# Kernel optimization log

Hardware: AMD Instinct MI355X
Metric: run time of the kernel (lower is better)

The kernel has to match this reference:

```python
import jax, jax.numpy as jnp
import numpy as np

N, E, H, HEADS, L, B = 16000, 256000, 192, 4, 4, 8
C = H // HEADS
VN, VE, T = 32, 8, 1000


def _sin_emb(t, dim):
    half = dim // 2
    freqs = jnp.exp(-np.log(10000.0) * jnp.arange(half, dtype=jnp.float32) / half)
    ang = t.astype(jnp.float32)[:, None] * freqs[None, :]
    return jnp.concatenate([jnp.sin(ang), jnp.cos(ang)], axis=-1)


def _ln(x, g, b, eps=1e-5):
    mu = jnp.mean(x, -1, keepdims=True)
    var = jnp.mean(jnp.square(x - mu), -1, keepdims=True)
    return (x - mu) * jax.lax.rsqrt(var + eps) * g + b


def setup_inputs():
    key = jax.random.key(0)
    ks = iter(jax.random.split(key, 64))
    p = lambda shape, s=0.02: jax.random.normal(next(ks), shape, jnp.float32) * s
    inp = {}
    inp['node_emb'] = p((VN, H))
    inp['edge_emb'] = p((VE, H))
    inp['time_w1'] = p((H, H)); inp['time_b1'] = jnp.zeros((H,), jnp.float32)
    inp['time_w2'] = p((H, H)); inp['time_b2'] = jnp.zeros((H,), jnp.float32)
    inp['mask_emb'] = p((2, H))
    inp['wq'] = p((L, H, H)); inp['bq'] = jnp.zeros((L, H), jnp.float32)
    inp['wk'] = p((L, H, H)); inp['bk'] = jnp.zeros((L, H), jnp.float32)
    inp['wv'] = p((L, H, H)); inp['bv'] = jnp.zeros((L, H), jnp.float32)
    inp['we'] = p((L, H, H))
    inp['wskip'] = p((L, H, H)); inp['bskip'] = jnp.zeros((L, H), jnp.float32)
    inp['wbeta'] = p((L, 3 * H))
    inp['ln_g'] = jnp.ones((L, H), jnp.float32); inp['ln_b'] = jnp.zeros((L, H), jnp.float32)
    inp['node_out_w'] = p((H, VN)); inp['node_out_b'] = jnp.zeros((VN,), jnp.float32)
    inp['edge_w1'] = p((4 * H, H)); inp['edge_b1'] = jnp.zeros((H,), jnp.float32)
    inp['edge_w2'] = p((H, VE)); inp['edge_b2'] = jnp.zeros((VE,), jnp.float32)
    inp['node_type'] = jax.random.randint(next(ks), (N,), 0, VN)
    inp['edge_type'] = jax.random.randint(next(ks), (E,), 0, VE)
    inp['edge_index'] = jax.random.randint(next(ks), (2, E), 0, N)
    inp['edit_mask'] = jax.random.randint(next(ks), (N,), 0, 2, dtype=jnp.int32)
    inp['node_batch'] = jnp.sort(jax.random.randint(next(ks), (N,), 0, B))
    inp['t_graph'] = jax.random.randint(next(ks), (B,), 1, T)
    return inp


def reference(node_emb, edge_emb, time_w1, time_b1, time_w2, time_b2, mask_emb,
              wq, bq, wk, bk, wv, bv, we, wskip, bskip, wbeta, ln_g, ln_b,
              node_out_w, node_out_b, edge_w1, edge_b1, edge_w2, edge_b2,
              node_type, edge_type, edge_index, edit_mask, node_batch, t_graph):
    src, dst = edge_index[0], edge_index[1]
    # time embedding: sinusoidal -> Linear -> SiLU -> Linear  => [B, H]
    t_vec = jax.nn.silu(_sin_emb(t_graph, H) @ time_w1 + time_b1) @ time_w2 + time_b2
    t_node = t_vec[node_batch]              # [N, H]
    t_edge = t_vec[node_batch[src]]         # [E, H]
    x = node_emb[node_type] + t_node + mask_emb[edit_mask]
    edge_attr = edge_emb[edge_type] + t_edge
    scale = 1.0 / np.sqrt(C)
    for l in range(L):
        q = (x @ wq[l] + bq[l]).reshape(N, HEADS, C)
        k = (x @ wk[l] + bk[l]).reshape(N, HEADS, C)
        v = (x @ wv[l] + bv[l]).reshape(N, HEADS, C)
        e = (edge_attr @ we[l]).reshape(E, HEADS, C)
        kj = k[src] + e                                   # [E, heads, C]
        score = jnp.sum(q[dst] * kj, axis=-1) * scale      # [E, heads]
        m = jax.ops.segment_max(score, dst, num_segments=N)
        ex = jnp.exp(score - m[dst])
        denom = jax.ops.segment_sum(ex, dst, num_segments=N)
        alpha = ex / denom[dst]
        msg = (v[src] + e) * alpha[..., None]              # [E, heads, C]
        out = jax.ops.segment_sum(msg, dst, num_segments=N).reshape(N, H)
        xr = x @ wskip[l] + bskip[l]
        beta = jax.nn.sigmoid(jnp.concatenate([out, xr, out - xr], -1) @ wbeta[l])[:, None]
        h = beta * xr + (1.0 - beta) * out
        x = _ln(x + h, ln_g[l], ln_b[l])
    node_logits = x @ node_out_w + node_out_b
    edge_feat = jnp.concatenate([x[src], x[dst], edge_attr, t_edge], -1)  # [E, 4H]
    edge_logits = jax.nn.silu(edge_feat @ edge_w1 + edge_b1) @ edge_w2 + edge_b2
    return node_logits, edge_logits
```

## Files before the change

### kernel.cpp

```cpp
#include <hip/hip_runtime.h>
#include <hip/hip_bf16.h>
#include <math.h>

#define NN 16000
#define NPAD 16128
#define NE 256000
#define H 192
#define RP 256
#define KVR 512
#define NL 4
#define NBATCH 8
#define VEt 8
#define HH (H*H)
#define EML 16

typedef __hip_bfloat16 bf16;
typedef unsigned short u16;
typedef unsigned char u8;
typedef unsigned int u32;
typedef __attribute__((ext_vector_type(8))) short bfrag_t;
typedef __attribute__((ext_vector_type(4))) float facc_t;
typedef __attribute__((ext_vector_type(4))) float f4;
typedef __attribute__((ext_vector_type(2))) unsigned int u32x2;

__device__ __forceinline__ bf16 f2b(float v){ return __float2bfloat16(v); }

__device__ __forceinline__ unsigned enc8sw(float x){
    unsigned u = __float_as_uint(x);
    unsigned s = (u >> 24) & 0x80u;
    float ax = fabsf(x);
    if(ax >= 448.f) return s | 0x7Eu;
    if(ax < 0.015625f){
        int q = (int)rintf(ax * 512.f);
        return s | (unsigned)q;
    }
    unsigned au = u & 0x7FFFFFFFu;
    unsigned lsb = (au >> 20) & 1u;
    au += 0x7FFFFu + lsb;
    unsigned E = (au >> 23) - 127u;
    unsigned M = (au >> 20) & 7u;
    if((int)E > 8) return s | 0x7Eu;
    return s | ((E + 7u) << 3) | M;
}
__device__ __forceinline__ unsigned enc8(float x){
#if __has_builtin(__builtin_amdgcn_cvt_pk_fp8_f32)
    return (u32)__builtin_amdgcn_cvt_pk_fp8_f32(x, x, 0, false) & 0xFFu;
#else
    return enc8sw(x);
#endif
}
template<int SEL>
__device__ __forceinline__ float dec8s(u32 w){
#if __has_builtin(__builtin_amdgcn_cvt_f32_fp8)
    return __builtin_amdgcn_cvt_f32_fp8((int)w, SEL);
#else
    unsigned v = (w >> (SEL*8)) & 0xFFu;
    unsigned e = (v >> 3) & 15u, m = v & 7u;
    float mag = e ? __builtin_ldexpf((float)(8u + m), (int)e - 10)
                  : __builtin_ldexpf((float)m, -9);
    return (v & 0x80u) ? -mag : mag;
#endif
}
__device__ __forceinline__ float frcp(float x){
#if __has_builtin(__builtin_amdgcn_rcpf)
    return __builtin_amdgcn_rcpf(x);
#else
    return 1.f/x;
#endif
}

__global__ void k_sentinel(float* __restrict__ out, float v){ out[0] = v; }

__global__ void k_transpose(const float* __restrict__ wq, const float* __restrict__ wk,
                            const float* __restrict__ wv, const float* __restrict__ wsk,
                            const float* __restrict__ w1, u16* __restrict__ wt){
    int mat = blockIdx.x;
    const float* src;
    if(mat < 4)       src = wq  + (size_t)mat*HH;
    else if(mat < 8)  src = wk  + (size_t)(mat-4)*HH;
    else if(mat < 12) src = wv  + (size_t)(mat-8)*HH;
    else if(mat < 16) src = wsk + (size_t)(mat-12)*HH;
    else              src = w1  + (size_t)(mat-16)*HH;
    u16* dst = wt + (size_t)mat*HH;
    const int slice = HH/8;
    int base = blockIdx.y*slice;
    for(int i = base + threadIdx.x; i < base + slice; i += blockDim.x){
        int k = i / H, n = i % H;
        bf16 b = f2b(src[i]);
        dst[n*H + k] = *(u16*)&b;
    }
}

__global__ void k_tvec(const int* __restrict__ tg, const float* __restrict__ w1,
                       const float* __restrict__ b1, const float* __restrict__ w2,
                       const float* __restrict__ b2, float* __restrict__ tvec){
    int b = blockIdx.x, j = threadIdx.x;
    __shared__ float emb[H], h1[H];
    float t = (float)tg[b];
    if(j < 96){
        float fr = __expf(-logf(10000.0f) * (float)j / 96.0f);
        float ang = t * fr;
        emb[j]      = sinf(ang);
        emb[j + 96] = cosf(ang);
    }
    __syncthreads();
    float acc = b1[j];
    for(int k = 0; k < H; k++) acc += emb[k] * w1[k*H + j];
    h1[j] = acc / (1.f + __expf(-acc));
    __syncthreads();
    float acc2 = b2[j];
    for(int k = 0; k < H; k++) acc2 += h1[k] * w2[k*H + j];
    tvec[b*H + j] = acc2;
}

__global__ void k_init_x(const float* __restrict__ nemb, const float* __restrict__ memb,
                         const float* __restrict__ tvec, const int* __restrict__ ntype,
                         const int* __restrict__ emask, const int* __restrict__ nbatch,
                         float* __restrict__ x, u16* __restrict__ xb){
    int idx = blockIdx.x*blockDim.x + threadIdx.x;
    if(idx >= NN*H) return;
    int n = idx / H, c = idx % H;
    float v = nemb[(size_t)ntype[n]*H + c] + tvec[nbatch[n]*H + c]
            + memb[(size_t)emask[n]*H + c];
    x[idx] = v;
    bf16 b = f2b(v); xb[idx] = *(u16*)&b;
}

__global__ void k_zero_i(int* __restrict__ p, int n){
    int i = blockIdx.x*blockDim.x + threadIdx.x;
    if(i < n) p[i] = 0;
}
__global__ void k_count(const int* __restrict__ edst, int* __restrict__ cnt){
    int e = blockIdx.x*blockDim.x + threadIdx.x;
    if(e < NE) atomicAdd(&cnt[edst[e]], 1);
}
__global__ __launch_bounds__(1024) void k_scan(const int* __restrict__ cnt,
                                               int* __restrict__ ofs, int* __restrict__ cur){
    __shared__ int wsum[16];
    __shared__ int carry_s;
    int tid = threadIdx.x, lane = tid & 63, w = tid >> 6;
    if(tid == 0) carry_s = 0;
    __syncthreads();
    for(int base = 0; base < NN; base += 1024){
        int idx = base + tid;
        int v = (idx < NN) ? cnt[idx] : 0;
        int sc = v;
        #pragma unroll
        for(int o = 1; o < 64; o <<= 1){
            int t = __shfl_up(sc, o);
            if(lane >= o) sc += t;
        }
        if(lane == 63) wsum[w] = sc;
        __syncthreads();
        if(w == 0){
            int ws = (lane < 16) ? wsum[lane] : 0;
            #pragma unroll
            for(int o = 1; o < 16; o <<= 1){
                int t = __shfl_up(ws, o);
                if(lane >= o) ws += t;
            }
            if(lane < 16) wsum[lane] = ws;
        }
        __syncthreads();
        int wbase = (w > 0) ? wsum[w-1] : 0;
        int c = carry_s;
        int excl = c + wbase + sc - v;
        if(idx < NN){ ofs[idx] = excl; cur[idx] = excl; }
        __syncthreads();
        if(tid == 0) carry_s = c + wsum[15];
        __syncthreads();
    }
    if(threadIdx.x == 0) ofs[NN] = carry_s;
}
__global__ void k_scatter(const int* __restrict__ esrc, const int* __restrict__ edst,
                          const int* __restrict__ etype, const int* __restrict__ nbatch,
                          int* __restrict__ cur, int2* __restrict__ spair){
    int e = blockIdx.x*blockDim.x + threadIdx.x;
    if(e >= NE) return;
    int s = esrc[e], d = edst[e];
    int pos = atomicAdd(&cur[d], 1);
    int2 se; se.x = s; se.y = nbatch[s]*VEt + etype[e];
    spair[pos] = se;
}

__global__ void k_etab(const float* __restrict__ eemb, const float* __restrict__ tvec,
                       const float* __restrict__ we, u16* __restrict__ etab){
    int blk = blockIdx.x;
    int l = blk >> 6, idx = blk & 63, b = idx >> 3, et = idx & 7;
    int c = threadIdx.x;
    __shared__ float a[H];
    a[c] = eemb[et*H + c] + tvec[b*H + c];
    __syncthreads();
    float acc = 0.f;
    const float* w = we + (size_t)l*HH;
    for(int k = 0; k < H; k++) acc += a[k] * w[k*H + c];
    bf16 bv = f2b(acc);
    etab[(size_t)blk*256 + (c/3)*4 + (c%3)] = *(u16*)&bv;
}

__global__ void k_ctab(const float* __restrict__ eemb, const float* __restrict__ tvec,
                       const float* __restrict__ w1, const float* __restrict__ b1,
                       float* __restrict__ ctab){
    int idx = blockIdx.x, b = idx >> 3, et = idx & 7;
    int c = threadIdx.x;
    __shared__ float a[H];
    a[c] = eemb[et*H + c] + tvec[b*H + c];
    __syncthreads();
    float acc = b1[c];
    for(int k = 0; k < H; k++){
        acc += a[k]          * w1[(size_t)(2*H + k)*H + c];
        acc += tvec[b*H + k] * w1[(size_t)(3*H + k)*H + c];
    }
    ctab[(size_t)idx*RP + (c/3)*4 + (c%3)] = acc;
}

struct GemmP {
    const u16* wt[4];
    const float* bias[4];
    void* out[4];
    int obf[4];
};
__global__ __launch_bounds__(256) void k_gemm(const u16* __restrict__ A, GemmP P){
    int oi = blockIdx.y / 3, nt = blockIdx.y % 3;
    const u16* Wt = P.wt[oi];
    const float* bias = P.bias[oi];
    int wave = threadIdx.x >> 6, lane = threadIdx.x & 63;
    int quad = lane >> 4, l16 = lane & 15;
    int m0 = blockIdx.x*256 + wave*64;
    int n0 = nt*64;
    facc_t acc[4][4];
    #pragma unroll
    for(int i = 0; i < 4; i++)
        #pragma unroll
        for(int j = 0; j < 4; j++){ acc[i][j][0]=0.f; acc[i][j][1]=0.f; acc[i][j][2]=0.f; acc[i][j][3]=0.f; }
    #pragma unroll
    for(int kc = 0; kc < 6; kc++){
        int kb = kc*32 + quad*8;
        bfrag_t af[4], bg[4];
        #pragma unroll
        for(int i = 0; i < 4; i++) af[i] = *(const bfrag_t*)(A  + (size_t)(m0 + i*16 + l16)*H + kb);
        #pragma unroll
        for(int j = 0; j < 4; j++) bg[j] = *(const bfrag_t*)(Wt + (size_t)(n0 + j*16 + l16)*H + kb);
        #pragma unroll
        for(int i = 0; i < 4; i++)
            #pragma unroll
            for(int j = 0; j < 4; j++)
                acc[i][j] = __builtin_amdgcn_mfma_f32_16x16x32_bf16(af[i], bg[j], acc[i][j], 0, 0, 0);
    }
    float bv[4];
    #pragma unroll
    for(int j = 0; j < 4; j++) bv[j] = bias ? bias[n0 + j*16 + l16] : 0.f;
    int mode = P.obf[oi];
    if(mode != 0){
        u8* out = (u8*)P.out[oi];
        int rstride = (mode == 2) ? RP : KVR;
        int mult    = (mode == 2) ? 4  : 8;
        int koff    = (mode == 4) ? 4  : 0;
        int byteoff[4];
        #pragma unroll
        for(int j = 0; j < 4; j++){
            int c = n0 + j*16 + l16;
            byteoff[j] = (c/3)*mult + (c%3) + koff;
        }
        #pragma unroll
        for(int i = 0; i < 4; i++){
            int rb = m0 + i*16 + quad*4;
            #pragma unroll
            for(int r = 0; r < 4; r++){
                int row = rb + r;
                if(row < NN){
                    #pragma unroll
                    for(int j = 0; j < 4; j++)
                        out[(size_t)row*rstride + byteoff[j]] = (u8)enc8(acc[i][j][r] + bv[j]);
                }
            }
        }
    } else {
        float* out = (float*)P.out[oi];
        #pragma unroll
        for(int i = 0; i < 4; i++){
            int rb = m0 + i*16 + quad*4;
            #pragma unroll
            for(int r = 0; r < 4; r++){
                int row = rb + r;
                if(row < NN){
                    #pragma unroll
                    for(int j = 0; j < 4; j++)
                        out[(size_t)row*H + n0 + j*16 + l16] = acc[i][j][r] + bv[j];
                }
            }
        }
    }
}

__global__ __launch_bounds__(256) void k_attn(
    const float* __restrict__ Q, const u8* __restrict__ KVb,
    const float* __restrict__ XR,
    const u16* __restrict__ etab, const int* __restrict__ ofs,
    const int2* __restrict__ spair,
    const float* __restrict__ wb, const float* __restrict__ lng, const float* __restrict__ lnb,
    float* __restrict__ x, u16* __restrict__ xb)
{
    int n = blockIdx.x*4 + (threadIdx.x >> 6);
    int lane = threadIdx.x & 63;
    int ch = lane*3;
    size_t base = (size_t)n*H + ch;
    const float scale = 0.14433756729740646f;
    float q0 = Q[base], q1 = Q[base+1], q2 = Q[base+2];
    int p0 = ofs[n], p1 = ofs[n+1];
    float lac[4]  = {0.f,0.f,0.f,0.f};
    float ac0[4]  = {0.f,0.f,0.f,0.f};
    float ac1[4]  = {0.f,0.f,0.f,0.f};
    float ac2[4]  = {0.f,0.f,0.f,0.f};
    const u8* etb = (const u8*)etab;
    int p = p0;
    for(; p + 3 < p1; p += 4){
        int s[4], ei[4];
        #pragma unroll
        for(int t = 0; t < 4; t++){ int2 se = spair[p+t]; s[t] = se.x; ei[t] = se.y; }
        u32x2 kv[4], ew[4];
        #pragma unroll
        for(int t = 0; t < 4; t++){
            kv[t] = *(const u32x2*)(KVb + (size_t)s[t]*KVR + lane*8);
            ew[t] = *(const u32x2*)(etb + (size_t)ei[t]*KVR + lane*8);
        }
        float e0[4], e1[4], e2[4], tt[4];
        #pragma unroll
        for(int t = 0; t < 4; t++){
            e0[t] = __uint_as_float(ew[t].x << 16);
            e1[t] = __uint_as_float(ew[t].x & 0xffff0000u);
            e2[t] = __uint_as_float(ew[t].y << 16);
            tt[t] = q0*(dec8s<0>(kv[t].x)+e0[t]) + q1*(dec8s<1>(kv[t].x)+e1[t])
                  + q2*(dec8s<2>(kv[t].x)+e2[t]);
        }
        #pragma unroll
        for(int o = 1; o <= 8; o <<= 1){
            #pragma unroll
            for(int t = 0; t < 4; t++) tt[t] += __shfl_xor(tt[t], o);
        }
        #pragma unroll
        for(int t = 0; t < 4; t++){
            float sc = fminf(fmaxf(tt[t]*scale, -60.f), 60.f);
            float pw = __expf(sc);
            lac[t] += pw;
            ac0[t] += pw*(dec8s<0>(kv[t].y)+e0[t]);
            ac1[t] += pw*(dec8s<1>(kv[t].y)+e1[t]);
            ac2[t] += pw*(dec8s<2>(kv[t].y)+e2[t]);
        }
    }
    for(; p < p1; p++){
        int2 se = spair[p];
        u32x2 kvA = *(const u32x2*)(KVb + (size_t)se.x*KVR + lane*8);
        u32x2 ewA = *(const u32x2*)(etb + (size_t)se.y*KVR + lane*8);
        float e0A = __uint_as_float(ewA.x << 16);
        float e1A = __uint_as_float(ewA.x & 0xffff0000u);
        float e2A = __uint_as_float(ewA.y << 16);
        float tA = q0*(dec8s<0>(kvA.x)+e0A) + q1*(dec8s<1>(kvA.x)+e1A) + q2*(dec8s<2>(kvA.x)+e2A);
        tA += __shfl_xor(tA,1); tA += __shfl_xor(tA,2); tA += __shfl_xor(tA,4); tA += __shfl_xor(tA,8);
        float sc = fminf(fmaxf(tA*scale, -60.f), 60.f);
        float pw = __expf(sc);
        lac[0] += pw;
        ac0[0] += pw*(dec8s<0>(kvA.y)+e0A);
        ac1[0] += pw*(dec8s<1>(kvA.y)+e1A);
        ac2[0] += pw*(dec8s<2>(kvA.y)+e2A);
    }
    float l  = (lac[0]+lac[1]) + (lac[2]+lac[3]);
    float a0 = (ac0[0]+ac0[1]) + (ac0[2]+ac0[3]);
    float a1 = (ac1[0]+ac1[1]) + (ac1[2]+ac1[3]);
    float a2 = (ac2[0]+ac2[1]) + (ac2[2]+ac2[3]);
    float inv = (p1 > p0) ? 1.f/l : 0.f;
    float o0 = a0*inv, o1 = a1*inv, o2 = a2*inv;
    float xr0 = XR[base], xr1 = XR[base+1], xr2 = XR[base+2];
    float sd = o0*wb[ch]  + o1*wb[ch+1]  + o2*wb[ch+2]
             + xr0*wb[H+ch] + xr1*wb[H+ch+1] + xr2*wb[H+ch+2]
             + (o0-xr0)*wb[2*H+ch] + (o1-xr1)*wb[2*H+ch+1] + (o2-xr2)*wb[2*H+ch+2];
    sd += __shfl_xor(sd,1); sd += __shfl_xor(sd,2); sd += __shfl_xor(sd,4);
    sd += __shfl_xor(sd,8); sd += __shfl_xor(sd,16); sd += __shfl_xor(sd,32);
    float beta = 1.f/(1.f + __expf(-sd));
    float h0 = beta*xr0 + (1.f-beta)*o0;
    float h1 = beta*xr1 + (1.f-beta)*o1;
    float h2 = beta*xr2 + (1.f-beta)*o2;
    float y0 = x[base] + h0, y1 = x[base+1] + h1, y2 = x[base+2] + h2;
    float s3 = y0 + y1 + y2;
    s3 += __shfl_xor(s3,1); s3 += __shfl_xor(s3,2); s3 += __shfl_xor(s3,4);
    s3 += __shfl_xor(s3,8); s3 += __shfl_xor(s3,16); s3 += __shfl_xor(s3,32);
    float mean = s3 * (1.f/H);
    float d0 = y0-mean, d1 = y1-mean, d2 = y2-mean;
    float v3 = d0*d0 + d1*d1 + d2*d2;
    v3 += __shfl_xor(v3,1); v3 += __shfl_xor(v3,2); v3 += __shfl_xor(v3,4);
    v3 += __shfl_xor(v3,8); v3 += __shfl_xor(v3,16); v3 += __shfl_xor(v3,32);
    float rs = rsqrtf(v3*(1.f/H) + 1e-5f);
    float z0 = d0*rs*lng[ch]   + lnb[ch];
    float z1 = d1*rs*lng[ch+1] + lnb[ch+1];
    float z2 = d2*rs*lng[ch+2] + lnb[ch+2];
    x[base] = z0; x[base+1] = z1; x[base+2] = z2;
    bf16 t0 = f2b(z0), t1 = f2b(z1), t2 = f2b(z2);
    xb[base] = *(u16*)&t0; xb[base+1] = *(u16*)&t1; xb[base+2] = *(u16*)&t2;
}

__global__ void k_nodeout(const float* __restrict__ x, const float* __restrict__ w,
                          const float* __restrict__ b, float* __restrict__ out){
    int j = threadIdx.x & 31;
    int n = blockIdx.x*8 + (threadIdx.x >> 5);
    float acc = b[j];
    const float* xr = x + (size_t)n*H;
    for(int k = 0; k < H; k++) acc += xr[k] * w[k*32 + j];
    out[(size_t)n*32 + j] = acc;
}

__global__ __launch_bounds__(256) void k_edgemlp(
    const int* __restrict__ esrc, const int* __restrict__ edst, const int* __restrict__ etype,
    const int* __restrict__ nb,
    const u8* __restrict__ xs1, const u8* __restrict__ xd1, const float* __restrict__ ctab,
    const float* __restrict__ w2, const float* __restrict__ b2p, float* __restrict__ out)
{
    int wid = blockIdx.x*4 + (threadIdx.x >> 6);
    int lane = threadIdx.x & 63;
    int ch = lane*3;
    float w2r[3][8];
    #pragma unroll
    for(int t = 0; t < 3; t++)
        #pragma unroll
        for(int j = 0; j < 8; j++) w2r[t][j] = w2[(ch+t)*8 + j];
    int jout = (lane&1)*4 + (lane&2) + ((lane&4)>>2);
    float bo = (lane < 8) ? b2p[jout] : 0.f;
    int b0 = lane & 1, b1 = lane & 2, b2m = lane & 4;
    int e0 = wid*EML;
    for(int eb = e0; eb < e0 + EML; eb += 2){
        int sX = esrc[eb],   dX = edst[eb];
        int sY = esrc[eb+1], dY = edst[eb+1];
        int ctX = nb[sX]*VEt + etype[eb];
        int ctY = nb[sY]*VEt + etype[eb+1];
        u32 awX = *(const u32*)(xs1 + (size_t)sX*RP + lane*4);
        u32 awY = *(const u32*)(xs1 + (size_t)sY*RP + lane*4);
        u32 bwX = *(const u32*)(xd1 + (size_t)dX*RP + lane*4);
        u32 bwY = *(const u32*)(xd1 + (size_t)dY*RP + lane*4);
        f4  cfX = *(const f4*)(ctab + (size_t)ctX*RP + lane*4);
        f4  cfY = *(const f4*)(ctab + (size_t)ctY*RP + lane*4);
        float hX0, hX1, hX2, hY0, hY1, hY2;
        { float v = dec8s<0>(awX)+dec8s<0>(bwX)+cfX.x; hX0 = v*frcp(1.f+__expf(-v)); }
        { float v = dec8s<1>(awX)+dec8s<1>(bwX)+cfX.y; hX1 = v*frcp(1.f+__expf(-v)); }
        { float v = dec8s<2>(awX)+dec8s<2>(bwX)+cfX.z; hX2 = v*frcp(1.f+__expf(-v)); }
        { float v = dec8s<0>(awY)+dec8s<0>(bwY)+cfY.x; hY0 = v*frcp(1.f+__expf(-v)); }
        { float v = dec8s<1>(awY)+dec8s<1>(bwY)+cfY.y; hY1 = v*frcp(1.f+__expf(-v)); }
        { float v = dec8s<2>(awY)+dec8s<2>(bwY)+cfY.z; hY2 = v*frcp(1.f+__expf(-v)); }
        float pjX[8], pjY[8];
        #pragma unroll
        for(int j = 0; j < 8; j++){
            pjX[j] = hX0*w2r[0][j] + hX1*w2r[1][j] + hX2*w2r[2][j];
            pjY[j] = hY0*w2r[0][j] + hY1*w2r[1][j] + hY2*w2r[2][j];
        }
        float v4X[4], v4Y[4];
        #pragma unroll
        for(int t = 0; t < 4; t++){
            float sX4 = b0 ? pjX[t] : pjX[t+4];
            float kX4 = b0 ? pjX[t+4] : pjX[t];
            v4X[t] = kX4 + __shfl_xor(sX4, 1);
            float sY4 = b0 ? pjY[t] : pjY[t+4];
            float kY4 = b0 ? pjY[t+4] : pjY[t];
            v4Y[t] = kY4 + __shfl_xor(sY4, 1);
        }
        float v2X[2], v2Y[2];
        #pragma unroll
        for(int t = 0; t < 2; t++){
            float sX2 = b1 ? v4X[t] : v4X[t+2];
            float kX2 = b1 ? v4X[t+2] : v4X[t];
            v2X[t] = kX2 + __shfl_xor(sX2, 2);
            float sY2 = b1 ? v4Y[t] : v4Y[t+2];
            float kY2 = b1 ? v4Y[t+2] : v4Y[t];
            v2Y[t] = kY2 + __shfl_xor(sY2, 2);
        }
        float v1X, v1Y;
        {
            float sX1 = b2m ? v2X[0] : v2X[1];
            float kX1 = b2m ? v2X[1] : v2X[0];
            v1X = kX1 + __shfl_xor(sX1, 4);
            float sY1 = b2m ? v2Y[0] : v2Y[1];
            float kY1 = b2m ? v2Y[1] : v2Y[0];
            v1Y = kY1 + __shfl_xor(sY1, 4);
        }
        v1X += __shfl_xor(v1X, 8);  v1Y += __shfl_xor(v1Y, 8);
        v1X += __shfl_xor(v1X, 16); v1Y += __shfl_xor(v1Y, 16);
        v1X += __shfl_xor(v1X, 32); v1Y += __shfl_xor(v1Y, 32);
        if(lane < 8){
            out[(size_t)eb*8 + jout]     = v1X + bo;
            out[(size_t)(eb+1)*8 + jout] = v1Y + bo;
        }
    }
}

extern "C" void kernel_launch(void* const* d_in, const int* in_sizes, int n_in,
                              void* d_out, int out_size, void* d_ws, size_t ws_size,
                              hipStream_t stream)
{
    {
        int bad = -1;
        if(n_in != 31) bad = 100;
        else {
            const int chk_idx[9] = {0, 7, 16, 21, 23, 26, 27, 29, 30};
            const int chk_sz [9] = {32*H, NL*HH, NL*3*H, 4*HH, H*8, NE, 2*NE, NN, NBATCH};
            for(int i = 0; i < 9; i++) if(in_sizes[chk_idx[i]] != chk_sz[i]){ bad = chk_idx[i]; break; }
        }
        if(bad >= 0){ k_sentinel<<<1,1,0,stream>>>((float*)d_out, 20000.f + 256.f*bad); return; }
        if(out_size != NN*32 + NE*8){ k_sentinel<<<1,1,0,stream>>>((float*)d_out, 30000.f); return; }
    }

    const float* node_emb = (const float*)d_in[0];
    const float* edge_emb = (const float*)d_in[1];
    const float* time_w1  = (const float*)d_in[2];
    const float* time_b1  = (const float*)d_in[3];
    const float* time_w2  = (const float*)d_in[4];
    const float* time_b2  = (const float*)d_in[5];
    const float* mask_emb = (const float*)d_in[6];
    const float* wq       = (const float*)d_in[7];
    const float* bq       = (const float*)d_in[8];
    const float* wk       = (const float*)d_in[9];
    const float* bk       = (const float*)d_in[10];
    const float* wv       = (const float*)d_in[11];
    const float* bv       = (const float*)d_in[12];
    const float* we       = (const float*)d_in[13];
    const float* wskip    = (const float*)d_in[14];
    const float* bskip    = (const float*)d_in[15];
    const float* wbeta    = (const float*)d_in[16];
    const float* ln_g     = (const float*)d_in[17];
    const float* ln_b     = (const float*)d_in[18];
    const float* now      = (const float*)d_in[19];
    const float* nob      = (const float*)d_in[20];
    const float* ew1      = (const float*)d_in[21];
    const float* eb1      = (const float*)d_in[22];
    const float* ew2      = (const float*)d_in[23];
    const float* eb2      = (const float*)d_in[24];
    const int* node_type  = (const int*)d_in[25];
    const int* edge_type  = (const int*)d_in[26];
    const int* edge_index = (const int*)d_in[27];
    const int* edit_mask  = (const int*)d_in[28];
    const int* node_batch = (const int*)d_in[29];
    const int* t_graph    = (const int*)d_in[30];
    const int* esrc = edge_index;
    const int* edst = edge_index + NE;

    char* wsb = (char*)d_ws;
    size_t off = 0;
    auto take = [&](size_t bytes) -> char* {
        char* r = wsb + off;
        off += (bytes + 255) & ~(size_t)255;
        return r;
    };
    float* tvec = (float*)take((size_t)NBATCH*H*4);
    float* x    = (float*)take((size_t)NN*H*4);
    u16*   xb   = (u16*)  take((size_t)NPAD*H*2);
    float* Q    = (float*)take((size_t)NN*H*4);
    u8*    KVb  = (u8*)   take((size_t)NN*KVR);
    float* XR   = (float*)take((size_t)NN*H*4);
    u8*    xs1  = (u8*)   take((size_t)NN*RP);
    u8*    xd1  = (u8*)   take((size_t)NN*RP);
    u16*   etab = (u16*)  take((size_t)NL*64*KVR);
    float* ctab = (float*)take((size_t)64*RP*4);
    u16*   wt   = (u16*)  take((size_t)18*HH*2);
    int* cnt    = (int*)  take((size_t)(NN+1)*4);
    int* offa   = (int*)  take((size_t)(NN+1)*4);
    int* cur    = (int*)  take((size_t)(NN+1)*4);
    int2* spair = (int2*) take((size_t)NE*8);

    if(ws_size < off){
        k_sentinel<<<1,1,0,stream>>>((float*)d_out, 10000.f + (float)(ws_size >> 20));
        return;
    }

    k_transpose<<<dim3(18, 8), 256, 0, stream>>>(wq, wk, wv, wskip, ew1, wt);
    k_tvec<<<NBATCH, H, 0, stream>>>(t_graph, time_w1, time_b1, time_w2, time_b2, tvec);
    k_init_x<<<(NN*H + 255)/256, 256, 0, stream>>>(node_emb, mask_emb, tvec, node_type,
                                                   edit_mask, node_batch, x, xb);
    k_zero_i<<<(NN + 255)/256, 256, 0, stream>>>(cnt, NN);
    k_count<<<NE/256, 256, 0, stream>>>(edst, cnt);
    k_scan<<<1, 1024, 0, stream>>>(cnt, offa, cur);
    k_scatter<<<NE/256, 256, 0, stream>>>(esrc, edst, edge_type, node_batch, cur, spair);
    k_etab<<<NL*64, H, 0, stream>>>(edge_emb, tvec, we, etab);
    k_ctab<<<64, H, 0, stream>>>(edge_emb, tvec, ew1, eb1, ctab);

    for(int l = 0; l < NL; l++){
        GemmP P;
        P.wt[0] = wt + (size_t)(0  + l)*HH;  P.bias[0] = bq   + (size_t)l*H;  P.out[0] = Q;   P.obf[0] = 0;
        P.wt[1] = wt + (size_t)(4  + l)*HH;  P.bias[1] = bk   + (size_t)l*H;  P.out[1] = KVb; P.obf[1] = 3;
        P.wt[2] = wt + (size_t)(8  + l)*HH;  P.bias[2] = bv   + (size_t)l*H;  P.out[2] = KVb; P.obf[2] = 4;
        P.wt[3] = wt + (size_t)(12 + l)*HH;  P.bias[3] = bskip+ (size_t)l*H;  P.out[3] = XR;  P.obf[3] = 0;
        k_gemm<<<dim3(63, 12), 256, 0, stream>>>(xb, P);
        k_attn<<<NN/4, 256, 0, stream>>>(Q, KVb, XR, etab + (size_t)l*64*256, offa, spair,
                                         wbeta + (size_t)l*3*H, ln_g + (size_t)l*H,
                                         ln_b + (size_t)l*H, x, xb);
    }
    {
        GemmP P;
        P.wt[0] = wt + (size_t)16*HH; P.bias[0] = nullptr; P.out[0] = xs1; P.obf[0] = 2;
        P.wt[1] = wt + (size_t)17*HH; P.bias[1] = nullptr; P.out[1] = xd1; P.obf[1] = 2;
        P.wt[2] = P.wt[0]; P.bias[2] = nullptr; P.out[2] = xs1; P.obf[2] = 2;
        P.wt[3] = P.wt[0]; P.bias[3] = nullptr; P.out[3] = xs1; P.obf[3] = 2;
        k_gemm<<<dim3(63, 6), 256, 0, stream>>>(xb, P);
    }
    k_nodeout<<<NN/8, 256, 0, stream>>>(x, now, nob, (float*)d_out);
    k_edgemlp<<<NE/(4*EML), 256, 0, stream>>>(esrc, edst, edge_type, node_batch, xs1, xd1, ctab,
                                              ew2, eb2, (float*)d_out + (size_t)NN*32);
}
```

Measured before the change: 537.6 us.

## Use bf16 MFMA for node output projection and edge MLP second layer

The node output projection now runs as a bf16 MFMA GEMM over the bf16 copy of x, replacing the per-thread fp32 dot-product loop. In the edge MLP, hidden activations are staged as bf16 in shared memory and projected to 8 outputs with MFMA against a padded, pre-transposed w2, replacing the shuffle-based reduction tree. Both weight matrices are transposed to bf16 in the existing transpose kernel. This lowers ALU and shuffle work, but adds bf16 rounding of the hidden activations and the weights, and the edge kernel gains a shared-memory buffer and a barrier.

After: 517.6 us. 1.04x faster.

```diff
diff --git a/kernel.cpp b/kernel.cpp
--- a/kernel.cpp
+++ b/kernel.cpp
@@ -73,21 +73,43 @@
 
 __global__ void k_transpose(const float* __restrict__ wq, const float* __restrict__ wk,
                             const float* __restrict__ wv, const float* __restrict__ wsk,
-                            const float* __restrict__ w1, u16* __restrict__ wt){
+                            const float* __restrict__ w1, const float* __restrict__ now,
+                            const float* __restrict__ ew2, u16* __restrict__ wt){
     int mat = blockIdx.x;
-    const float* src;
-    if(mat < 4)       src = wq  + (size_t)mat*HH;
-    else if(mat < 8)  src = wk  + (size_t)(mat-4)*HH;
-    else if(mat < 12) src = wv  + (size_t)(mat-8)*HH;
-    else if(mat < 16) src = wsk + (size_t)(mat-12)*HH;
-    else              src = w1  + (size_t)(mat-16)*HH;
-    u16* dst = wt + (size_t)mat*HH;
-    const int slice = HH/8;
-    int base = blockIdx.y*slice;
-    for(int i = base + threadIdx.x; i < base + slice; i += blockDim.x){
-        int k = i / H, n = i % H;
-        bf16 b = f2b(src[i]);
-        dst[n*H + k] = *(u16*)&b;
+    if(mat < 18){
+        const float* src;
+        if(mat < 4)       src = wq  + (size_t)mat*HH;
+        else if(mat < 8)  src = wk  + (size_t)(mat-4)*HH;
+        else if(mat < 12) src = wv  + (size_t)(mat-8)*HH;
+        else if(mat < 16) src = wsk + (size_t)(mat-12)*HH;
+        else              src = w1  + (size_t)(mat-16)*HH;
+        u16* dst = wt + (size_t)mat*HH;
+        const int slice = HH/8;
+        int base = blockIdx.y*slice;
+        for(int i = base + threadIdx.x; i < base + slice; i += blockDim.x){
+            int k = i / H, n = i % H;
+            bf16 b = f2b(src[i]);
+            dst[n*H + k] = *(u16*)&b;
+        }
+    } else if(mat == 18){
+        u16* dst = wt + (size_t)18*HH;
+        const int slice = (32*192)/8;
+        int base = blockIdx.y*slice;
+        for(int i = base + threadIdx.x; i < base + slice; i += blockDim.x){
+            int k = i >> 5, n = i & 31;
+            bf16 b = f2b(now[i]);
+            dst[n*192 + k] = *(u16*)&b;
+        }
+    } else {
+        u16* dst = wt + (size_t)18*HH + 32*192;
+        const int slice = (16*192)/8;
+        int base = blockIdx.y*slice;
+        for(int i = base + threadIdx.x; i < base + slice; i += blockDim.x){
+            int k = i >> 4, n = i & 15;
+            float v = (n < 8) ? ew2[k*8 + n] : 0.f;
+            bf16 b = f2b(v);
+            dst[n*192 + k] = *(u16*)&b;
+        }
     }
 }
 
@@ -398,39 +420,70 @@
     xb[base] = *(u16*)&t0; xb[base+1] = *(u16*)&t1; xb[base+2] = *(u16*)&t2;
 }
 
-__global__ void k_nodeout(const float* __restrict__ x, const float* __restrict__ w,
-                          const float* __restrict__ b, float* __restrict__ out){
-    int j = threadIdx.x & 31;
-    int n = blockIdx.x*8 + (threadIdx.x >> 5);
-    float acc = b[j];
-    const float* xr = x + (size_t)n*H;
-    for(int k = 0; k < H; k++) acc += xr[k] * w[k*32 + j];
-    out[(size_t)n*32 + j] = acc;
+__global__ __launch_bounds__(256) void k_nodeout(const u16* __restrict__ A, const u16* __restrict__ Wt,
+                                                 const float* __restrict__ b, float* __restrict__ out){
+    int wave = threadIdx.x >> 6, lane = threadIdx.x & 63;
+    int quad = lane >> 4, l16 = lane & 15;
+    int m0 = blockIdx.x*256 + wave*64;
+    facc_t acc[4][2];
+    #pragma unroll
+    for(int i = 0; i < 4; i++)
+        #pragma unroll
+        for(int j = 0; j < 2; j++){ acc[i][j][0]=0.f; acc[i][j][1]=0.f; acc[i][j][2]=0.f; acc[i][j][3]=0.f; }
+    #pragma unroll
+    for(int kc = 0; kc < 6; kc++){
+        int kb = kc*32 + quad*8;
+        bfrag_t af[4], bg[2];
+        #pragma unroll
+        for(int i = 0; i < 4; i++) af[i] = *(const bfrag_t*)(A  + (size_t)(m0 + i*16 + l16)*H + kb);
+        #pragma unroll
+        for(int j = 0; j < 2; j++) bg[j] = *(const bfrag_t*)(Wt + (size_t)(j*16 + l16)*H + kb);
+        #pragma unroll
+        for(int i = 0; i < 4; i++)
+            #pragma unroll
+            for(int j = 0; j < 2; j++)
+                acc[i][j] = __builtin_amdgcn_mfma_f32_16x16x32_bf16(af[i], bg[j], acc[i][j], 0, 0, 0);
+    }
+    float bv[2];
+    #pragma unroll
+    for(int j = 0; j < 2; j++) bv[j] = b[j*16 + l16];
+    #pragma unroll
+    for(int i = 0; i < 4; i++){
+        int rb = m0 + i*16 + quad*4;
+        #pragma unroll
+        for(int r = 0; r < 4; r++){
+            int row = rb + r;
+            if(row < NN){
+                #pragma unroll
+                for(int j = 0; j < 2; j++)
+                    out[(size_t)row*32 + j*16 + l16] = acc[i][j][r] + bv[j];
+            }
+        }
+    }
 }
 
 __global__ __launch_bounds__(256) void k_edgemlp(
     const int* __restrict__ esrc, const int* __restrict__ edst, const int* __restrict__ etype,
     const int* __restrict__ nb,
     const u8* __restrict__ xs1, const u8* __restrict__ xd1, const float* __restrict__ ctab,
-    const float* __restrict__ w2, const float* __restrict__ b2p, float* __restrict__ out)
+    const u16* __restrict__ w2t, const float* __restrict__ b2p, float* __restrict__ out)
 {
-    int wid = blockIdx.x*4 + (threadIdx.x >> 6);
+    __shared__ u16 hbuf[4][16][200];
+    int wave = threadIdx.x >> 6;
     int lane = threadIdx.x & 63;
-    int ch = lane*3;
-    float w2r[3][8];
-    #pragma unroll
-    for(int t = 0; t < 3; t++)
-        #pragma unroll
-        for(int j = 0; j < 8; j++) w2r[t][j] = w2[(ch+t)*8 + j];
-    int jout = (lane&1)*4 + (lane&2) + ((lane&4)>>2);
-    float bo = (lane < 8) ? b2p[jout] : 0.f;
-    int b0 = lane & 1, b1 = lane & 2, b2m = lane & 4;
+    int l16 = lane & 15, quad = lane >> 4;
+    int wid = blockIdx.x*4 + wave;
     int e0 = wid*EML;
-    for(int eb = e0; eb < e0 + EML; eb += 2){
-        int sX = esrc[eb],   dX = edst[eb];
-        int sY = esrc[eb+1], dY = edst[eb+1];
-        int ctX = nb[sX]*VEt + etype[eb];
-        int ctY = nb[sY]*VEt + etype[eb+1];
+    bfrag_t bg[6];
+    #pragma unroll
+    for(int kc = 0; kc < 6; kc++)
+        bg[kc] = *(const bfrag_t*)(w2t + (size_t)l16*192 + kc*32 + quad*8);
+    for(int eb = 0; eb < EML; eb += 2){
+        int eX = e0 + eb, eY = e0 + eb + 1;
+        int sX = esrc[eX], dX = edst[eX];
+        int sY = esrc[eY], dY = edst[eY];
+        int ctX = nb[sX]*VEt + etype[eX];
+        int ctY = nb[sY]*VEt + etype[eY];
         u32 awX = *(const u32*)(xs1 + (size_t)sX*RP + lane*4);
         u32 awY = *(const u32*)(xs1 + (size_t)sY*RP + lane*4);
         u32 bwX = *(const u32*)(xd1 + (size_t)dX*RP + lane*4);
@@ -444,47 +497,27 @@
         { float v = dec8s<0>(awY)+dec8s<0>(bwY)+cfY.x; hY0 = v*frcp(1.f+__expf(-v)); }
         { float v = dec8s<1>(awY)+dec8s<1>(bwY)+cfY.y; hY1 = v*frcp(1.f+__expf(-v)); }
         { float v = dec8s<2>(awY)+dec8s<2>(bwY)+cfY.z; hY2 = v*frcp(1.f+__expf(-v)); }
-        float pjX[8], pjY[8];
-        #pragma unroll
-        for(int j = 0; j < 8; j++){
-            pjX[j] = hX0*w2r[0][j] + hX1*w2r[1][j] + hX2*w2r[2][j];
-            pjY[j] = hY0*w2r[0][j] + hY1*w2r[1][j] + hY2*w2r[2][j];
-        }
-        float v4X[4], v4Y[4];
-        #pragma unroll
-        for(int t = 0; t < 4; t++){
-            float sX4 = b0 ? pjX[t] : pjX[t+4];
-            float kX4 = b0 ? pjX[t+4] : pjX[t];
-            v4X[t] = kX4 + __shfl_xor(sX4, 1);
-            float sY4 = b0 ? pjY[t] : pjY[t+4];
-            float kY4 = b0 ? pjY[t+4] : pjY[t];
-            v4Y[t] = kY4 + __shfl_xor(sY4, 1);
-        }
-        float v2X[2], v2Y[2];
-        #pragma unroll
-        for(int t = 0; t < 2; t++){
-            float sX2 = b1 ? v4X[t] : v4X[t+2];
-            float kX2 = b1 ? v4X[t+2] : v4X[t];
-            v2X[t] = kX2 + __shfl_xor(sX2, 2);
-            float sY2 = b1 ? v4Y[t] : v4Y[t+2];
-            float kY2 = b1 ? v4Y[t+2] : v4Y[t];
-            v2Y[t] = kY2 + __shfl_xor(sY2, 2);
-        }
-        float v1X, v1Y;
-        {
-            float sX1 = b2m ? v2X[0] : v2X[1];
-            float kX1 = b2m ? v2X[1] : v2X[0];
-            v1X = kX1 + __shfl_xor(sX1, 4);
-            float sY1 = b2m ? v2Y[0] : v2Y[1];
-            float kY1 = b2m ? v2Y[1] : v2Y[0];
-            v1Y = kY1 + __shfl_xor(sY1, 4);
-        }
-        v1X += __shfl_xor(v1X, 8);  v1Y += __shfl_xor(v1Y, 8);
-        v1X += __shfl_xor(v1X, 16); v1Y += __shfl_xor(v1Y, 16);
-        v1X += __shfl_xor(v1X, 32); v1Y += __shfl_xor(v1Y, 32);
-        if(lane < 8){
-            out[(size_t)eb*8 + jout]     = v1X + bo;
-            out[(size_t)(eb+1)*8 + jout] = v1Y + bo;
+        u16* rowX = &hbuf[wave][eb][0];
+        u16* rowY = &hbuf[wave][eb+1][0];
+        bf16 x0 = f2b(hX0), x1 = f2b(hX1), x2 = f2b(hX2);
+        bf16 y0 = f2b(hY0), y1 = f2b(hY1), y2 = f2b(hY2);
+        rowX[lane*3+0] = *(u16*)&x0; rowX[lane*3+1] = *(u16*)&x1; rowX[lane*3+2] = *(u16*)&x2;
+        rowY[lane*3+0] = *(u16*)&y0; rowY[lane*3+1] = *(u16*)&y1; rowY[lane*3+2] = *(u16*)&y2;
+    }
+    __syncthreads();
+    facc_t acc;
+    acc[0]=0.f; acc[1]=0.f; acc[2]=0.f; acc[3]=0.f;
+    #pragma unroll
+    for(int kc = 0; kc < 6; kc++){
+        bfrag_t af = *(const bfrag_t*)&hbuf[wave][l16][kc*32 + quad*8];
+        acc = __builtin_amdgcn_mfma_f32_16x16x32_bf16(af, bg[kc], acc, 0, 0, 0);
+    }
+    if(l16 < 8){
+        float bo = b2p[l16];
+        #pragma unroll
+        for(int r = 0; r < 4; r++){
+            int e = e0 + quad*4 + r;
+            out[(size_t)e*8 + l16] = acc[r] + bo;
         }
     }
 }
@@ -556,7 +589,7 @@
     u8*    xd1  = (u8*)   take((size_t)NN*RP);
     u16*   etab = (u16*)  take((size_t)NL*64*KVR);
     float* ctab = (float*)take((size_t)64*RP*4);
-    u16*   wt   = (u16*)  take((size_t)18*HH*2);
+    u16*   wt   = (u16*)  take((size_t)(18*HH + 32*192 + 16*192)*2);
     int* cnt    = (int*)  take((size_t)(NN+1)*4);
     int* offa   = (int*)  take((size_t)(NN+1)*4);
     int* cur    = (int*)  take((size_t)(NN+1)*4);
@@ -567,7 +600,10 @@
         return;
     }
 
-    k_transpose<<<dim3(18, 8), 256, 0, stream>>>(wq, wk, wv, wskip, ew1, wt);
+    u16* w32t = wt + (size_t)18*HH;
+    u16* w2t  = w32t + 32*192;
+
+    k_transpose<<<dim3(20, 8), 256, 0, stream>>>(wq, wk, wv, wskip, ew1, now, ew2, wt);
     k_tvec<<<NBATCH, H, 0, stream>>>(t_graph, time_w1, time_b1, time_w2, time_b2, tvec);
     k_init_x<<<(NN*H + 255)/256, 256, 0, stream>>>(node_emb, mask_emb, tvec, node_type,
                                                    edit_mask, node_batch, x, xb);
@@ -597,7 +633,7 @@
         P.wt[3] = P.wt[0]; P.bias[3] = nullptr; P.out[3] = xs1; P.obf[3] = 2;
         k_gemm<<<dim3(63, 6), 256, 0, stream>>>(xb, P);
     }
-    k_nodeout<<<NN/8, 256, 0, stream>>>(x, now, nob, (float*)d_out);
+    k_nodeout<<<63, 256, 0, stream>>>(xb, w32t, nob, (float*)d_out);
     k_edgemlp<<<NE/(4*EML), 256, 0, stream>>>(esrc, edst, edge_type, node_batch, xs1, xd1, ctab,
-                                              ew2, eb2, (float*)d_out + (size_t)NN*32);
-}
+                                              w2t, eb2, (float*)d_out + (size_t)NN*32);
+}
```
